# Kernel optimization log

Hardware: AMD Instinct MI355X
Metric: run time of the kernel (lower is better)

## Reference

```python
import math
import jax, jax.numpy as jnp
import numpy as np

B, L, E, H = 8, 1024, 512, 8
HD = E // H  # head_dim = 64
P = 2 * L - 1  # relative position length


def setup_inputs() -> dict:
    key = jax.random.key(0)
    ks = jax.random.split(key, 9)
    s = 0.02  # xavier-ish scale for params
    return {
        "x": jax.random.normal(ks[0], (B, L, E), jnp.float32),
        "pos_embs": jax.random.normal(ks[1], (1, P, E), jnp.float32),
        "in_proj_weight": jax.random.normal(ks[2], (3 * E, E), jnp.float32) * s,
        "linear_pos_w": jax.random.normal(ks[3], (E, E), jnp.float32) * s,
        "out_proj_w": jax.random.normal(ks[4], (E, E), jnp.float32) * s,
        "out_proj_b": jnp.zeros((E,), jnp.float32),
        "pos_bias_u": jax.random.normal(ks[5], (HD, H), jnp.float32) * s,
        "pos_bias_v": jax.random.normal(ks[6], (HD, H), jnp.float32) * s,
    }


def rel_shift(t):
    # Transformer-XL relative shift: pad/reshape/slice trick.
    b, h, q, p = t.shape  # p = 2*klen - 1
    t = jnp.pad(t, ((0, 0), (0, 0), (0, 0), (1, 0)))
    t = t.reshape(b, h, p + 1, q)[:, :, 1:, :].reshape(b, h, q, p)
    return t[..., : p // 2 + 1]  # (b, h, q, klen)


def reference(x, pos_embs, in_proj_weight, linear_pos_w, out_proj_w, out_proj_b,
              pos_bias_u, pos_bias_v):
    bsz, qlen, _ = x.shape
    scale = 1.0 / math.sqrt(E)  # note: 1/sqrt(embed_dim), not head_dim

    # fused qkv projection; torch chunks along the last dim of (B,L,H,3*HD)
    proj = (x @ in_proj_weight.T).reshape(bsz, qlen, H, 3 * HD)
    q, k, v = jnp.split(proj, 3, axis=-1)  # each (B,L,H,HD)

    # positional keys
    p_k = (pos_embs @ linear_pos_w.T).reshape(-1, H, HD)  # (P,H,HD)

    # pos_bias_u is stored (HD,H) and .view(H,HD)'d in torch -> plain reshape
    u = pos_bias_u.reshape(H, HD)
    vb = pos_bias_v.reshape(H, HD)

    matrix_ac = jnp.einsum('bqhd,bkhd->bhqk', (q + u) * scale, k)
    matrix_bd = jnp.einsum('bqhd,phd->bhqp', (q + vb) * scale, p_k)
    matrix_bd = rel_shift(matrix_bd)  # (B,H,L,L)

    attn = jax.nn.softmax((matrix_ac + matrix_bd).astype(jnp.float32), axis=-1)

    ctx = jnp.einsum('bhqk,bkhd->bqhd', attn, v).reshape(bsz, qlen, E)
    out = ctx @ out_proj_w.T + out_proj_b
    return out, attn
```

## Files before the change

kernel.cpp:

```cpp
#include <hip/hip_runtime.h>
#include <math.h>

#define BB 8
#define LL 1024
#define EE 512
#define HH 8
#define HD 64
#define PP 2047

static constexpr float SCALE = 0.04419417382415922f;

typedef __bf16 bf16x8 __attribute__((ext_vector_type(8)));
typedef float f32x4 __attribute__((ext_vector_type(4)));
typedef unsigned short u16;
typedef u16 u16x8 __attribute__((ext_vector_type(8)));
typedef u16 u16x4 __attribute__((ext_vector_type(4)));

#define MFMA16(a, b, c) __builtin_amdgcn_mfma_f32_16x16x32_bf16(a, b, c, 0, 0, 0)

static __device__ __forceinline__ unsigned short f2bfbits(float f) {
    union { float f; unsigned u; } v; v.f = f;
    unsigned r = v.u + 0x7fffu + ((v.u >> 16) & 1u);
    return (unsigned short)(r >> 16);
}
static __device__ __forceinline__ float bfbits2f(unsigned short b) {
    union { unsigned u; float f; } v; v.u = ((unsigned)b) << 16;
    return v.f;
}

static __device__ __forceinline__ u16x8 cvt8(float4 lo, float4 hi) {
    u16x8 r;
    r[0] = f2bfbits(lo.x); r[1] = f2bfbits(lo.y);
    r[2] = f2bfbits(lo.z); r[3] = f2bfbits(lo.w);
    r[4] = f2bfbits(hi.x); r[5] = f2bfbits(hi.y);
    r[6] = f2bfbits(hi.z); r[7] = f2bfbits(hi.w);
    return r;
}

static __device__ __forceinline__ void gload_lds16(const u16* g, u16* l) {
    __builtin_amdgcn_global_load_lds(
        (const __attribute__((address_space(1))) unsigned int*)g,
        (__attribute__((address_space(3))) unsigned int*)l, 16, 0, 0);
}

__global__ __launch_bounds__(256) void cast_all(
    const float* __restrict__ x, const float* __restrict__ pe,
    const float* __restrict__ ipw, const float* __restrict__ lpw,
    const float* __restrict__ opw,
    u16* __restrict__ Xb, u16* __restrict__ Pb, u16* __restrict__ Wqb,
    u16* __restrict__ Wpb, u16* __restrict__ Wob)
{
    size_t e = ((size_t)blockIdx.x * 256 + threadIdx.x) * 8;
    const float* src; u16* dst; size_t off;
    if (e < 4194304)      { src = x;   dst = Xb;  off = e; }
    else if (e < 5242368) { src = pe;  dst = Pb;  off = e - 4194304; }
    else if (e < 6028800) { src = ipw; dst = Wqb; off = e - 5242368; }
    else if (e < 6290944) { src = lpw; dst = Wpb; off = e - 6028800; }
    else if (e < 6553088) { src = opw; dst = Wob; off = e - 6290944; }
    else return;
    float4 lo = *(const float4*)&src[off];
    float4 hi = *(const float4*)&src[off + 4];
    *(u16x8*)&dst[off] = cvt8(lo, hi);
}

template<bool CLAMP>
static __device__ __forceinline__ void gemm128b(
    const u16* __restrict__ Ab, const u16* __restrict__ Bb,
    int m0, int n0, int amax, u16* As, u16* Bs, f32x4 (&acc)[4][4])
{
    const int tid = threadIdx.x;
    const int w = tid >> 6, lane = tid & 63;
    const int g = lane >> 4, c16 = lane & 15;
    const int wr = w >> 1, wc = w & 1;

#pragma unroll
    for (int i = 0; i < 4; i++)
#pragma unroll
        for (int j = 0; j < 4; j++) acc[i][j] = (f32x4){0.f, 0.f, 0.f, 0.f};

    int arow[4], brow[4], cs8[4], ldsu[4];
#pragma unroll
    for (int j = 0; j < 4; j++) {
        int U = j * 256 + tid;
        int row = U >> 3, cu = U & 7;
        cs8[j] = (cu ^ (row & 7)) * 8;
        int ar = m0 + row;
        if (CLAMP) ar = ar > amax ? amax : ar;
        arow[j] = ar;
        brow[j] = n0 + row;
        ldsu[j] = (j * 256 + (w << 6)) * 8;
    }

    for (int kt = 0; kt < EE; kt += 64) {
#pragma unroll
        for (int j = 0; j < 4; j++) {
            gload_lds16(Ab + (size_t)arow[j] * EE + kt + cs8[j], As + ldsu[j]);
            gload_lds16(Bb + (size_t)brow[j] * EE + kt + cs8[j], Bs + ldsu[j]);
        }
        __syncthreads();
#pragma unroll
        for (int kk = 0; kk < 2; kk++) {
            bf16x8 av[4], bv[4];
#pragma unroll
            for (int mt = 0; mt < 4; mt++) {
                int r0 = wr * 64 + mt * 16 + c16;
                av[mt] = *(const bf16x8*)&As[r0 * 64 + (((kk * 4 + g) ^ (r0 & 7)) << 3)];
            }
#pragma unroll
            for (int nt = 0; nt < 4; nt++) {
                int r0 = wc * 64 + nt * 16 + c16;
                bv[nt] = *(const bf16x8*)&Bs[r0 * 64 + (((kk * 4 + g) ^ (r0 & 7)) << 3)];
            }
#pragma unroll
            for (int mt = 0; mt < 4; mt++)
#pragma unroll
                for (int nt = 0; nt < 4; nt++)
                    acc[mt][nt] = MFMA16(av[mt], bv[nt], acc[mt][nt]);
        }
        __syncthreads();
    }
}

__global__ __launch_bounds__(256) void qkv_kernel(
    const u16* __restrict__ xb,
    const u16* __restrict__ wq,
    const float* __restrict__ ubias,
    const float* __restrict__ vbias,
    unsigned short* __restrict__ Qu,
    unsigned short* __restrict__ Qv,
    unsigned short* __restrict__ Kw,
    unsigned short* __restrict__ Vt)
{
    __shared__ u16 As[128 * 64];
    __shared__ u16 Bs[128 * 64];
    const int m0 = blockIdx.y * 128, n0 = blockIdx.x * 128;
    f32x4 acc[4][4];
    gemm128b<false>(xb, wq, m0, n0, 0, As, Bs, acc);

    const int tid = threadIdx.x;
    const int w = tid >> 6, lane = tid & 63;
    const int g = lane >> 4, c16 = lane & 15;
    const int wr = w >> 1, wc = w & 1;

#pragma unroll
    for (int mt = 0; mt < 4; mt++) {
#pragma unroll
        for (int r = 0; r < 4; r++) {
            int m = m0 + wr * 64 + mt * 16 + g * 4 + r;
            int b = m >> 10, l = m & 1023;
#pragma unroll
            for (int nt = 0; nt < 4; nt++) {
                int n = n0 + wc * 64 + nt * 16 + c16;
                int h = n / 192;
                int rr = n - h * 192;
                int cls = rr >> 6;
                int d = rr & 63;
                float v = acc[mt][nt][r];
                if (cls == 0) {
                    size_t idx = ((size_t)(b * HH + h) * LL + l) * HD + d;
                    Qu[idx] = f2bfbits((v + ubias[h * 64 + d]) * SCALE);
                    Qv[idx] = f2bfbits((v + vbias[h * 64 + d]) * SCALE);
                } else if (cls == 1) {
                    Kw[((size_t)(b * HH + h) * LL + l) * HD + d] = f2bfbits(v);
                } else {
                    Vt[((size_t)(b * HH + h) * HD + d) * LL + l] = f2bfbits(v);
                }
            }
        }
    }
}

__global__ __launch_bounds__(256) void posk_kernel(
    const u16* __restrict__ peb,
    const u16* __restrict__ wp,
    unsigned short* __restrict__ pko)
{
    __shared__ u16 As[128 * 64];
    __shared__ u16 Bs[128 * 64];
    const int m0 = blockIdx.y * 128, n0 = blockIdx.x * 128;
    f32x4 acc[4][4];
    gemm128b<true>(peb, wp, m0, n0, PP - 1, As, Bs, acc);

    const int tid = threadIdx.x;
    const int w = tid >> 6, lane = tid & 63;
    const int g = lane >> 4, c16 = lane & 15;
    const int wr = w >> 1, wc = w & 1;

#pragma unroll
    for (int mt = 0; mt < 4; mt++) {
#pragma unroll
        for (int r = 0; r < 4; r++) {
            int p = m0 + wr * 64 + mt * 16 + g * 4 + r;
            if (p >= PP) continue;
#pragma unroll
            for (int nt = 0; nt < 4; nt++) {
                int n = n0 + wc * 64 + nt * 16 + c16;
                int h = n >> 6, d = n & 63;
                pko[((size_t)h * PP + p) * HD + d] = f2bfbits(acc[mt][nt][r]);
            }
        }
    }
}

__global__ __launch_bounds__(256) void outproj_kernel(
    const u16* __restrict__ ctxb,
    const u16* __restrict__ wo,
    const float* __restrict__ bias,
    float* __restrict__ out)
{
    __shared__ u16 As[128 * 64];
    __shared__ u16 Bs[128 * 64];
    const int m0 = blockIdx.y * 128, n0 = blockIdx.x * 128;
    f32x4 acc[4][4];
    gemm128b<false>(ctxb, wo, m0, n0, 0, As, Bs, acc);

    const int tid = threadIdx.x;
    const int w = tid >> 6, lane = tid & 63;
    const int g = lane >> 4, c16 = lane & 15;
    const int wr = w >> 1, wc = w & 1;

#pragma unroll
    for (int mt = 0; mt < 4; mt++) {
#pragma unroll
        for (int r = 0; r < 4; r++) {
            int m = m0 + wr * 64 + mt * 16 + g * 4 + r;
#pragma unroll
            for (int nt = 0; nt < 4; nt++) {
                int n = n0 + wc * 64 + nt * 16 + c16;
                out[(size_t)m * EE + n] = acc[mt][nt][r] + bias[n];
            }
        }
    }
}

__global__ __launch_bounds__(256, 3) void attn_kernel(
    const unsigned short* __restrict__ Qu, const unsigned short* __restrict__ Qv,
    const unsigned short* __restrict__ Kw, const unsigned short* __restrict__ Vt,
    const unsigned short* __restrict__ pk,
    float* __restrict__ attn,
    u16* __restrict__ ctxb)
{
    const int b = blockIdx.z, h = blockIdx.y, q0 = blockIdx.x * 16;
    const int tid = threadIdx.x;
    const int w = tid >> 6, lane = tid & 63;
    const int g = lane >> 4, c16 = lane & 15;
    const int bh = b * HH + h;

    __shared__ unsigned short BDG[4][16 * 152];
    __shared__ float SMmax[4][16];
    __shared__ float SMsum[4][16];
    __shared__ float CTX[4][16 * 68];

    const unsigned short* qub = Qu + ((size_t)bh * LL + q0 + c16) * HD + g * 8;
    const unsigned short* qvb = Qv + ((size_t)bh * LL + q0 + c16) * HD + g * 8;
    bf16x8 au0 = *(const bf16x8*)qub;
    bf16x8 au1 = *(const bf16x8*)(qub + 32);
    bf16x8 av0 = *(const bf16x8*)qvb;
    bf16x8 av1 = *(const bf16x8*)(qvb + 32);

    f32x4 lg[16];
#pragma unroll
    for (int t = 0; t < 16; t++) lg[t] = (f32x4){0.f, 0.f, 0.f, 0.f};

    const unsigned short* kbase  = Kw + (size_t)bh * LL * HD;
    const unsigned short* pkbase = pk + (size_t)h * PP * HD;

#pragma unroll
    for (int p = 0; p < 2; p++) {
        const int kp = w * 256 + p * 128;
        const int pstart = kp - q0 + 1008;
#pragma unroll
        for (int ct = 0; ct < 9; ct++) {
            int prow = pstart + ct * 16 + c16;
            prow = prow > (PP - 1) ? (PP - 1) : prow;
            const unsigned short* pb = pkbase + (size_t)prow * HD + g * 8;
            f32x4 acc = (f32x4){0.f, 0.f, 0.f, 0.f};
            acc = MFMA16(av0, *(const bf16x8*)pb, acc);
            acc = MFMA16(av1, *(const bf16x8*)(pb + 32), acc);
#pragma unroll
            for (int r = 0; r < 4; r++)
                BDG[w][(g * 4 + r) * 152 + ct * 16 + c16] = f2bfbits(acc[r]);
        }
#pragma unroll
        for (int jt = 0; jt < 8; jt++) {
            const unsigned short* kb = kbase + (size_t)(kp + jt * 16 + c16) * HD + g * 8;
            int t = p * 8 + jt;
            lg[t] = MFMA16(au0, *(const bf16x8*)kb, lg[t]);
            lg[t] = MFMA16(au1, *(const bf16x8*)(kb + 32), lg[t]);
        }
        __syncthreads();
#pragma unroll
        for (int jt = 0; jt < 8; jt++) {
            int t = p * 8 + jt;
#pragma unroll
            for (int r = 0; r < 4; r++) {
                int i = g * 4 + r;
                int c = jt * 16 + c16 - i + 15;
                lg[t][r] += bfbits2f(BDG[w][i * 152 + c]);
            }
        }
        __syncthreads();
    }

    float M[4], Sv[4], inv[4];
#pragma unroll
    for (int r = 0; r < 4; r++) {
        float m = lg[0][r];
#pragma unroll
        for (int t = 1; t < 16; t++) m = fmaxf(m, lg[t][r]);
        M[r] = m;
    }
#pragma unroll
    for (int off = 8; off >= 1; off >>= 1)
#pragma unroll
        for (int r = 0; r < 4; r++) M[r] = fmaxf(M[r], __shfl_xor(M[r], off, 16));
    if (c16 == 0) {
#pragma unroll
        for (int r = 0; r < 4; r++) SMmax[w][g * 4 + r] = M[r];
    }
    __syncthreads();
#pragma unroll
    for (int r = 0; r < 4; r++) {
        int row = g * 4 + r;
        M[r] = fmaxf(fmaxf(SMmax[0][row], SMmax[1][row]),
                     fmaxf(SMmax[2][row], SMmax[3][row]));
        Sv[r] = 0.f;
    }
#pragma unroll
    for (int t = 0; t < 16; t++)
#pragma unroll
        for (int r = 0; r < 4; r++) {
            float e = __expf(lg[t][r] - M[r]);
            lg[t][r] = e;
            Sv[r] += e;
        }
#pragma unroll
    for (int off = 8; off >= 1; off >>= 1)
#pragma unroll
        for (int r = 0; r < 4; r++) Sv[r] += __shfl_xor(Sv[r], off, 16);
    if (c16 == 0) {
#pragma unroll
        for (int r = 0; r < 4; r++) SMsum[w][g * 4 + r] = Sv[r];
    }
    __syncthreads();
#pragma unroll
    for (int r = 0; r < 4; r++) {
        int row = g * 4 + r;
        inv[r] = 1.0f / (SMsum[0][row] + SMsum[1][row] + SMsum[2][row] + SMsum[3][row]);
    }

    float* arow = attn + (size_t)bh * LL * LL;
#pragma unroll
    for (int t = 0; t < 16; t++)
#pragma unroll
        for (int r = 0; r < 4; r++) {
            float pr = lg[t][r] * inv[r];
            lg[t][r] = pr;
            arow[(size_t)(q0 + g * 4 + r) * LL + w * 256 + t * 16 + c16] = pr;
        }

    f32x4 cacc[4];
#pragma unroll
    for (int nt = 0; nt < 4; nt++) cacc[nt] = (f32x4){0.f, 0.f, 0.f, 0.f};

#pragma unroll
    for (int p = 0; p < 2; p++) {
        const int kp = w * 256 + p * 128;
        __syncthreads();
#pragma unroll
        for (int jt = 0; jt < 8; jt++) {
            int t = p * 8 + jt;
#pragma unroll
            for (int r = 0; r < 4; r++)
                BDG[w][(g * 4 + r) * 152 + jt * 16 + c16] = f2bfbits(lg[t][r]);
        }
        __syncthreads();
        bf16x8 pa[4];
#pragma unroll
        for (int kk = 0; kk < 4; kk++)
            pa[kk] = *(const bf16x8*)&BDG[w][c16 * 152 + kk * 32 + g * 8];
#pragma unroll
        for (int kk = 0; kk < 4; kk++) {
#pragma unroll
            for (int nt = 0; nt < 4; nt++) {
                const unsigned short* vb =
                    Vt + ((size_t)bh * HD + nt * 16 + c16) * LL + kp + kk * 32 + g * 8;
                cacc[nt] = MFMA16(pa[kk], *(const bf16x8*)vb, cacc[nt]);
            }
        }
    }

    __syncthreads();
#pragma unroll
    for (int nt = 0; nt < 4; nt++)
#pragma unroll
        for (int r = 0; r < 4; r++)
            CTX[w][(g * 4 + r) * 68 + nt * 16 + c16] = cacc[nt][r];
    __syncthreads();
    {
        int row = tid >> 4, d4 = (tid & 15) * 4;
        f32x4 s = *(const f32x4*)&CTX[0][row * 68 + d4];
        s += *(const f32x4*)&CTX[1][row * 68 + d4];
        s += *(const f32x4*)&CTX[2][row * 68 + d4];
        s += *(const f32x4*)&CTX[3][row * 68 + d4];
        u16x4 o;
        o[0] = f2bfbits(s[0]); o[1] = f2bfbits(s[1]);
        o[2] = f2bfbits(s[2]); o[3] = f2bfbits(s[3]);
        *(u16x4*)&ctxb[((size_t)b * LL + q0 + row) * EE + h * HD + d4] = o;
    }
}

extern "C" void kernel_launch(void* const* d_in, const int* in_sizes, int n_in,
                              void* d_out, int out_size, void* d_ws, size_t ws_size,
                              hipStream_t stream)
{
    const float* x   = (const float*)d_in[0];
    const float* pe  = (const float*)d_in[1];
    const float* ipw = (const float*)d_in[2];
    const float* lpw = (const float*)d_in[3];
    const float* opw = (const float*)d_in[4];
    const float* opb = (const float*)d_in[5];
    const float* pbu = (const float*)d_in[6];
    const float* pbv = (const float*)d_in[7];

    float* out  = (float*)d_out;
    float* attn = (float*)d_out + (size_t)BB * LL * EE;

    const size_t NQ = (size_t)BB * HH * LL * HD;
    u16* wsu  = (u16*)d_ws;
    u16* ctxb = wsu; wsu += (size_t)BB * LL * EE;
    u16* Qu   = wsu; wsu += NQ;
    u16* Qv   = wsu; wsu += NQ;
    u16* Kw   = wsu; wsu += NQ;
    u16* Vt   = wsu; wsu += NQ;
    u16* pkb  = wsu; wsu += (size_t)HH * PP * HD;
    u16* Xb   = wsu; wsu += 4194304;
    u16* Pb   = wsu; wsu += 1048064;
    u16* Wqb  = wsu; wsu += 786432;
    u16* Wpb  = wsu; wsu += 262144;
    u16* Wob  = wsu; wsu += 262144;

    cast_all<<<3200, 256, 0, stream>>>(x, pe, ipw, lpw, opw, Xb, Pb, Wqb, Wpb, Wob);
    qkv_kernel<<<dim3(12, 64), 256, 0, stream>>>(Xb, Wqb, pbu, pbv, Qu, Qv, Kw, Vt);
    posk_kernel<<<dim3(4, 16), 256, 0, stream>>>(Pb, Wpb, pkb);
    attn_kernel<<<dim3(64, 8, 8), 256, 0, stream>>>(Qu, Qv, Kw, Vt, pkb, attn, ctxb);
    outproj_kernel<<<dim3(4, 64), 256, 0, stream>>>(ctxb, opw ? Wob : Wob, opb, out);
}
```

Before: 541.2 us.

## Merge QKV and pos-key GEMMs, swizzle blocks per XCD, alias attention LDS

Merges the QKV projection and positional-key projection into one launch with a flat block index. Remaps block IDs in all GEMM and attention kernels so that consecutive blocks on the same XCD share rows or (batch, head) data, aiming for better L2 locality. The attention kernel aliases its per-wave BDG and CTX shared buffers to cut LDS usage and raises the occupancy hint from 3 to 4 blocks. Large attention and output stores become nontemporal to avoid polluting cache. Together these target launch overhead, cache misses and occupancy, at the cost of possible register pressure under the tighter launch bound.

```diff
diff --git a/kernel.cpp b/kernel.cpp
--- a/kernel.cpp
+++ b/kernel.cpp
@@ -121,7 +121,7 @@
     }
 }
 
-__global__ __launch_bounds__(256) void qkv_kernel(
+__global__ __launch_bounds__(256) void qkvpos_kernel(
     const u16* __restrict__ xb,
     const u16* __restrict__ wq,
     const float* __restrict__ ubias,
@@ -129,74 +129,66 @@
     unsigned short* __restrict__ Qu,
     unsigned short* __restrict__ Qv,
     unsigned short* __restrict__ Kw,
-    unsigned short* __restrict__ Vt)
+    unsigned short* __restrict__ Vt,
+    const u16* __restrict__ peb,
+    const u16* __restrict__ wp,
+    unsigned short* __restrict__ pko)
 {
     __shared__ u16 As[128 * 64];
     __shared__ u16 Bs[128 * 64];
-    const int m0 = blockIdx.y * 128, n0 = blockIdx.x * 128;
-    f32x4 acc[4][4];
-    gemm128b<false>(xb, wq, m0, n0, 0, As, Bs, acc);
-
+    const int bid = blockIdx.x;
     const int tid = threadIdx.x;
     const int w = tid >> 6, lane = tid & 63;
     const int g = lane >> 4, c16 = lane & 15;
     const int wr = w >> 1, wc = w & 1;
-
-#pragma unroll
-    for (int mt = 0; mt < 4; mt++) {
-#pragma unroll
-        for (int r = 0; r < 4; r++) {
-            int m = m0 + wr * 64 + mt * 16 + g * 4 + r;
-            int b = m >> 10, l = m & 1023;
-#pragma unroll
-            for (int nt = 0; nt < 4; nt++) {
-                int n = n0 + wc * 64 + nt * 16 + c16;
-                int h = n / 192;
-                int rr = n - h * 192;
-                int cls = rr >> 6;
-                int d = rr & 63;
-                float v = acc[mt][nt][r];
-                if (cls == 0) {
-                    size_t idx = ((size_t)(b * HH + h) * LL + l) * HD + d;
-                    Qu[idx] = f2bfbits((v + ubias[h * 64 + d]) * SCALE);
-                    Qv[idx] = f2bfbits((v + vbias[h * 64 + d]) * SCALE);
-                } else if (cls == 1) {
-                    Kw[((size_t)(b * HH + h) * LL + l) * HD + d] = f2bfbits(v);
-                } else {
-                    Vt[((size_t)(b * HH + h) * HD + d) * LL + l] = f2bfbits(v);
+    f32x4 acc[4][4];
+
+    if (bid < 768) {
+        const int xcd = bid & 7, j = bid >> 3;
+        const int m0 = (xcd * 8 + j / 12) * 128, n0 = (j % 12) * 128;
+        gemm128b<false>(xb, wq, m0, n0, 0, As, Bs, acc);
+#pragma unroll
+        for (int mt = 0; mt < 4; mt++) {
+#pragma unroll
+            for (int r = 0; r < 4; r++) {
+                int m = m0 + wr * 64 + mt * 16 + g * 4 + r;
+                int b = m >> 10, l = m & 1023;
+#pragma unroll
+                for (int nt = 0; nt < 4; nt++) {
+                    int n = n0 + wc * 64 + nt * 16 + c16;
+                    int h = n / 192;
+                    int rr = n - h * 192;
+                    int cls = rr >> 6;
+                    int d = rr & 63;
+                    float v = acc[mt][nt][r];
+                    if (cls == 0) {
+                        size_t idx = ((size_t)(b * HH + h) * LL + l) * HD + d;
+                        Qu[idx] = f2bfbits((v + ubias[h * 64 + d]) * SCALE);
+                        Qv[idx] = f2bfbits((v + vbias[h * 64 + d]) * SCALE);
+                    } else if (cls == 1) {
+                        Kw[((size_t)(b * HH + h) * LL + l) * HD + d] = f2bfbits(v);
+                    } else {
+                        Vt[((size_t)(b * HH + h) * HD + d) * LL + l] = f2bfbits(v);
+                    }
                 }
             }
         }
-    }
-}
-
-__global__ __launch_bounds__(256) void posk_kernel(
-    const u16* __restrict__ peb,
-    const u16* __restrict__ wp,
-    unsigned short* __restrict__ pko)
-{
-    __shared__ u16 As[128 * 64];
-    __shared__ u16 Bs[128 * 64];
-    const int m0 = blockIdx.y * 128, n0 = blockIdx.x * 128;
-    f32x4 acc[4][4];
-    gemm128b<true>(peb, wp, m0, n0, PP - 1, As, Bs, acc);
-
-    const int tid = threadIdx.x;
-    const int w = tid >> 6, lane = tid & 63;
-    const int g = lane >> 4, c16 = lane & 15;
-    const int wr = w >> 1, wc = w & 1;
-
-#pragma unroll
-    for (int mt = 0; mt < 4; mt++) {
-#pragma unroll
-        for (int r = 0; r < 4; r++) {
-            int p = m0 + wr * 64 + mt * 16 + g * 4 + r;
-            if (p >= PP) continue;
-#pragma unroll
-            for (int nt = 0; nt < 4; nt++) {
-                int n = n0 + wc * 64 + nt * 16 + c16;
-                int h = n >> 6, d = n & 63;
-                pko[((size_t)h * PP + p) * HD + d] = f2bfbits(acc[mt][nt][r]);
+    } else {
+        const int j = bid - 768;
+        const int m0 = (j >> 2) * 128, n0 = (j & 3) * 128;
+        gemm128b<true>(peb, wp, m0, n0, PP - 1, As, Bs, acc);
+#pragma unroll
+        for (int mt = 0; mt < 4; mt++) {
+#pragma unroll
+            for (int r = 0; r < 4; r++) {
+                int p = m0 + wr * 64 + mt * 16 + g * 4 + r;
+                if (p >= PP) continue;
+#pragma unroll
+                for (int nt = 0; nt < 4; nt++) {
+                    int n = n0 + wc * 64 + nt * 16 + c16;
+                    int h = n >> 6, d = n & 63;
+                    pko[((size_t)h * PP + p) * HD + d] = f2bfbits(acc[mt][nt][r]);
+                }
             }
         }
     }
@@ -210,7 +202,9 @@
 {
     __shared__ u16 As[128 * 64];
     __shared__ u16 Bs[128 * 64];
-    const int m0 = blockIdx.y * 128, n0 = blockIdx.x * 128;
+    const int bid = blockIdx.x;
+    const int xcd = bid & 7, j = bid >> 3;
+    const int m0 = (xcd * 8 + (j >> 2)) * 128, n0 = (j & 3) * 128;
     f32x4 acc[4][4];
     gemm128b<false>(ctxb, wo, m0, n0, 0, As, Bs, acc);
 
@@ -227,29 +221,33 @@
 #pragma unroll
             for (int nt = 0; nt < 4; nt++) {
                 int n = n0 + wc * 64 + nt * 16 + c16;
-                out[(size_t)m * EE + n] = acc[mt][nt][r] + bias[n];
-            }
-        }
-    }
-}
-
-__global__ __launch_bounds__(256, 3) void attn_kernel(
+                __builtin_nontemporal_store(acc[mt][nt][r] + bias[n],
+                                            &out[(size_t)m * EE + n]);
+            }
+        }
+    }
+}
+
+__global__ __launch_bounds__(256, 4) void attn_kernel(
     const unsigned short* __restrict__ Qu, const unsigned short* __restrict__ Qv,
     const unsigned short* __restrict__ Kw, const unsigned short* __restrict__ Vt,
     const unsigned short* __restrict__ pk,
     float* __restrict__ attn,
     u16* __restrict__ ctxb)
 {
-    const int b = blockIdx.z, h = blockIdx.y, q0 = blockIdx.x * 16;
+    const int bid = blockIdx.x;
+    const int xcd = bid & 7, jj = bid >> 3;
+    const int bh = xcd * 8 + (jj >> 6);
+    const int q0 = (jj & 63) * 16;
+    const int b = bh >> 3, h = bh & 7;
     const int tid = threadIdx.x;
     const int w = tid >> 6, lane = tid & 63;
     const int g = lane >> 4, c16 = lane & 15;
-    const int bh = b * HH + h;
-
-    __shared__ unsigned short BDG[4][16 * 152];
+
+    __shared__ __align__(16) unsigned char SH[4][4864];
     __shared__ float SMmax[4][16];
     __shared__ float SMsum[4][16];
-    __shared__ float CTX[4][16 * 68];
+    unsigned short* BDGw = (unsigned short*)SH[w];
 
     const unsigned short* qub = Qu + ((size_t)bh * LL + q0 + c16) * HD + g * 8;
     const unsigned short* qvb = Qv + ((size_t)bh * LL + q0 + c16) * HD + g * 8;
@@ -279,7 +277,7 @@
             acc = MFMA16(av1, *(const bf16x8*)(pb + 32), acc);
 #pragma unroll
             for (int r = 0; r < 4; r++)
-                BDG[w][(g * 4 + r) * 152 + ct * 16 + c16] = f2bfbits(acc[r]);
+                BDGw[(g * 4 + r) * 152 + ct * 16 + c16] = f2bfbits(acc[r]);
         }
 #pragma unroll
         for (int jt = 0; jt < 8; jt++) {
@@ -296,7 +294,7 @@
             for (int r = 0; r < 4; r++) {
                 int i = g * 4 + r;
                 int c = jt * 16 + c16 - i + 15;
-                lg[t][r] += bfbits2f(BDG[w][i * 152 + c]);
+                lg[t][r] += bfbits2f(BDGw[i * 152 + c]);
             }
         }
         __syncthreads();
@@ -356,7 +354,8 @@
         for (int r = 0; r < 4; r++) {
             float pr = lg[t][r] * inv[r];
             lg[t][r] = pr;
-            arow[(size_t)(q0 + g * 4 + r) * LL + w * 256 + t * 16 + c16] = pr;
+            __builtin_nontemporal_store(
+                pr, &arow[(size_t)(q0 + g * 4 + r) * LL + w * 256 + t * 16 + c16]);
         }
 
     f32x4 cacc[4];
@@ -372,13 +371,13 @@
             int t = p * 8 + jt;
 #pragma unroll
             for (int r = 0; r < 4; r++)
-                BDG[w][(g * 4 + r) * 152 + jt * 16 + c16] = f2bfbits(lg[t][r]);
+                BDGw[(g * 4 + r) * 152 + jt * 16 + c16] = f2bfbits(lg[t][r]);
         }
         __syncthreads();
         bf16x8 pa[4];
 #pragma unroll
         for (int kk = 0; kk < 4; kk++)
-            pa[kk] = *(const bf16x8*)&BDG[w][c16 * 152 + kk * 32 + g * 8];
+            pa[kk] = *(const bf16x8*)&BDGw[c16 * 152 + kk * 32 + g * 8];
 #pragma unroll
         for (int kk = 0; kk < 4; kk++) {
 #pragma unroll
@@ -391,18 +390,21 @@
     }
 
     __syncthreads();
-#pragma unroll
-    for (int nt = 0; nt < 4; nt++)
-#pragma unroll
-        for (int r = 0; r < 4; r++)
-            CTX[w][(g * 4 + r) * 68 + nt * 16 + c16] = cacc[nt][r];
+    {
+        float* CTXw = (float*)SH[w];
+#pragma unroll
+        for (int nt = 0; nt < 4; nt++)
+#pragma unroll
+            for (int r = 0; r < 4; r++)
+                CTXw[(g * 4 + r) * 68 + nt * 16 + c16] = cacc[nt][r];
+    }
     __syncthreads();
     {
         int row = tid >> 4, d4 = (tid & 15) * 4;
-        f32x4 s = *(const f32x4*)&CTX[0][row * 68 + d4];
-        s += *(const f32x4*)&CTX[1][row * 68 + d4];
-        s += *(const f32x4*)&CTX[2][row * 68 + d4];
-        s += *(const f32x4*)&CTX[3][row * 68 + d4];
+        f32x4 s = *(const f32x4*)&((const float*)SH[0])[row * 68 + d4];
+        s += *(const f32x4*)&((const float*)SH[1])[row * 68 + d4];
+        s += *(const f32x4*)&((const float*)SH[2])[row * 68 + d4];
+        s += *(const f32x4*)&((const float*)SH[3])[row * 68 + d4];
         u16x4 o;
         o[0] = f2bfbits(s[0]); o[1] = f2bfbits(s[1]);
         o[2] = f2bfbits(s[2]); o[3] = f2bfbits(s[3]);
@@ -441,8 +443,8 @@
     u16* Wob  = wsu; wsu += 262144;
 
     cast_all<<<3200, 256, 0, stream>>>(x, pe, ipw, lpw, opw, Xb, Pb, Wqb, Wpb, Wob);
-    qkv_kernel<<<dim3(12, 64), 256, 0, stream>>>(Xb, Wqb, pbu, pbv, Qu, Qv, Kw, Vt);
-    posk_kernel<<<dim3(4, 16), 256, 0, stream>>>(Pb, Wpb, pkb);
-    attn_kernel<<<dim3(64, 8, 8), 256, 0, stream>>>(Qu, Qv, Kw, Vt, pkb, attn, ctxb);
-    outproj_kernel<<<dim3(4, 64), 256, 0, stream>>>(ctxb, opw ? Wob : Wob, opb, out);
-}
+    qkvpos_kernel<<<832, 256, 0, stream>>>(Xb, Wqb, pbu, pbv, Qu, Qv, Kw, Vt,
+                                           Pb, Wpb, pkb);
+    attn_kernel<<<4096, 256, 0, stream>>>(Qu, Qv, Kw, Vt, pkb, attn, ctxb);
+    outproj_kernel<<<256, 256, 0, stream>>>(ctxb, Wob, opb, out);
+}
```

After: 523.3 us. 1.03x faster.
